# Kernel optimization log

Measured on AMD Instinct MI355X. Metric: run time of the kernel, lower is better.

Reference implementation:

```python
import jax, jax.numpy as jnp
import numpy as np

N_SITES = 1024
A_PER_SITE = 2
R_PER_ALLELE = 16
N_ALLELES = N_SITES * A_PER_SITE
N_READS = N_ALLELES * R_PER_ALLELE
C_IN, C, L = 16, 32, 150


def conv1d(x, w, stride=1, dilation=1, pad=2):
    return jax.lax.conv_general_dilated(
        x, w, (stride,), [(pad, pad)], rhs_dilation=(dilation,),
        dimension_numbers=('NCH', 'OIH', 'NCH'))


def reduce_slots(d, slots):
    # cumsum-diff segmented sum over dim 0, exactly as torch reduceSlots
    res = jnp.cumsum(d, axis=0)
    idx = jnp.cumsum(slots) - 1
    sel = res[idx]
    padded = jnp.concatenate([jnp.zeros_like(sel[:1]), sel[:-1]], axis=0)
    return sel - padded


def xattn(allele, site0, site1, wq, wk, wv, wo):
    # cross-attention: allele features query the two expanded site-feature streams
    q = jnp.einsum('oc,ncl->nol', wq, allele)
    kv = jnp.concatenate([site0, site1], axis=-1)  # [Na, C, 2*L']
    k = jnp.einsum('oc,ncl->nol', wk, kv)
    v = jnp.einsum('oc,ncl->nol', wv, kv)
    scores = jnp.einsum('ncl,ncm->nlm', q, k) / np.float32(np.sqrt(C))
    ctx = jnp.einsum('nlm,ncm->ncl', jax.nn.softmax(scores, axis=-1), v)
    return jnp.mean(allele + ctx, axis=-1) @ wo.T  # [Na, 2]


def setup_inputs():
    ks = jax.random.split(jax.random.key(0), 24)
    w = lambda i, shape: jax.random.normal(ks[i], shape, jnp.float32) * 0.05
    return {
        'tensors0': jax.random.normal(ks[0], (N_READS, C_IN, L), jnp.float32),
        'tensors1': jax.random.normal(ks[1], (N_READS, C_IN, L), jnp.float32),
        'conv0_w': w(2, (C, C_IN, 5)), 'conv1_w': w(3, (C, C_IN, 5)),
        'comp0_w': w(4, (C, C, 3)), 'comp1_w': w(5, (C, C, 3)), 'comp2_w': w(6, (C, C, 3)),
        'xq0': w(7, (C, C)), 'xk0': w(8, (C, C)), 'xv0': w(9, (C, C)), 'xo0': w(10, (2, C)),
        'xq1': w(11, (C, C)), 'xk1': w(12, (C, C)), 'xv1': w(13, (C, C)), 'xo1': w(14, (2, C)),
        'xq2': w(15, (C, C)), 'xk2': w(16, (C, C)), 'xv2': w(17, (C, C)), 'xo2': w(18, (2, C)),
        'comb_w': w(19, (C, 2 * C)), 'meta_w': w(20, (3, 2 * C)), 'meta_b': w(21, (3,)),
        'num_alleles_per_site': jnp.full((N_SITES,), A_PER_SITE, jnp.int32),
        'num_reads0': jnp.full((N_ALLELES,), R_PER_ALLELE, jnp.int32),
        'num_reads1': jnp.full((N_ALLELES,), R_PER_ALLELE, jnp.int32),
    }


def reference(tensors0, tensors1, conv0_w, conv1_w, comp0_w, comp1_w, comp2_w,
              xq0, xk0, xv0, xo0, xq1, xk1, xv1, xo1, xq2, xk2, xv2, xo2,
              comb_w, meta_w, meta_b, num_alleles_per_site, num_reads0, num_reads1):
    compressor = lambda x, w: jax.nn.relu(conv1d(x, w, stride=2, dilation=2, pad=2))

    def compress_and_predict(red_allele, comp_w, xw):
        cfa = compressor(red_allele, comp_w)                       # [Na, C, L']
        rfs = reduce_slots(red_allele, num_alleles_per_site)       # [Ns, C, L]
        cfs0 = compressor(rfs, comp_w)                             # [Ns, C, L']
        exp0 = jnp.repeat(cfs0, num_alleles_per_site, axis=0, total_repeat_length=N_ALLELES)
        cfs1 = reduce_slots(cfa, num_alleles_per_site)             # [Ns, C, L']
        exp1 = jnp.repeat(cfs1, num_alleles_per_site, axis=0, total_repeat_length=N_ALLELES)
        return xattn(cfa, exp0, exp1, *xw), (cfs0, cfs1)

    rc0 = jax.nn.relu(conv1d(tensors0, conv0_w, pad=2))            # [Nr, C, L]
    red0 = reduce_slots(rc0, num_reads0)                           # [Na, C, L]
    e0, _ = compress_and_predict(red0, comp0_w, (xq0, xk0, xv0, xo0))

    rc1 = jax.nn.relu(conv1d(tensors1, conv1_w, pad=2))
    red1 = reduce_slots(rc1, num_reads1)
    e1, _ = compress_and_predict(red1, comp1_w, (xq1, xk1, xv1, xo1))

    red2 = jax.nn.relu(jnp.einsum('oc,ncl->nol', comb_w, jnp.concatenate([red0, red1], axis=1)))
    e2, (s0, s1) = compress_and_predict(red2, comp2_w, (xq2, xk2, xv2, xo2))

    meta_feat = jnp.mean(jnp.concatenate([s0, s1], axis=1), axis=-1)  # [Ns, 2C]
    meta = jax.nn.softmax(meta_feat @ meta_w.T + meta_b, axis=-1)     # [Ns, 3]
    return (jnp.stack([e0, e1, e2]), meta)
```

## Files before the change

### kernel.cpp

```cpp
#include <hip/hip_runtime.h>
#include <math.h>

#define NS 1024
#define NA 2048
#define CIN 16
#define CC 32
#define LL 150
#define LC 75

typedef __attribute__((ext_vector_type(8))) short short8;
typedef __attribute__((ext_vector_type(4))) float float4v;

__device__ __forceinline__ unsigned short f2bf(float f) {
  unsigned int u = __float_as_uint(f);
  unsigned int r = (u + 0x7FFFu + ((u >> 16) & 1u)) >> 16;
  return (unsigned short)r;
}

__device__ __forceinline__ unsigned int pkbf(float lo, float hi) {
  return (unsigned int)f2bf(lo) | ((unsigned int)f2bf(hi) << 16);
}

__device__ __forceinline__ float bflo(unsigned int u) { return __uint_as_float(u << 16); }
__device__ __forceinline__ float bfhi(unsigned int u) { return __uint_as_float(u & 0xffff0000u); }

#if __has_builtin(__builtin_amdgcn_fdot2_f32_bf16)
typedef __attribute__((ext_vector_type(2))) __bf16 bf16x2;
__device__ __forceinline__ float bdot2(unsigned int a, unsigned int b, float c) {
  return __builtin_amdgcn_fdot2_f32_bf16(__builtin_bit_cast(bf16x2, a),
                                         __builtin_bit_cast(bf16x2, b), c, false);
}
#else
__device__ __forceinline__ float bdot2(unsigned int a, unsigned int b, float c) {
  return c + bflo(a) * bflo(b) + bfhi(a) * bfhi(b);
}
#endif

__global__ __launch_bounds__(256) void k_conv_sum_mfma(const float* __restrict__ x,
                                                       const float* __restrict__ w,
                                                       float* __restrict__ red) {
  __shared__ unsigned short xs[2][154 * 32];
  const int a = blockIdx.x;
  const int tid = threadIdx.x;
  const int lane = tid & 63;
  const int wv = tid >> 6;

  short8 afr[2][3];
  {
    const int mrow = lane & 15;
    const int h = lane >> 4;
    for (int mt = 0; mt < 2; ++mt) {
      const int c = mt * 16 + mrow;
      for (int s = 0; s < 3; ++s) {
        short8 f;
#pragma unroll
        for (int j = 0; j < 8; ++j) {
          int ic = 4 * h + (j >> 1);
          int tap = 2 * s + (j & 1);
          float wval = (tap < 5) ? w[c * 80 + ic * 5 + tap] : 0.f;
          f[j] = (short)f2bf(wval);
        }
        afr[mt][s] = f;
      }
    }
  }

  float4v sum[2][3];
#pragma unroll
  for (int mt = 0; mt < 2; ++mt)
#pragma unroll
    for (int nt = 0; nt < 3; ++nt) sum[mt][nt] = (float4v)(0.f);

  const int nbase = wv * 48;
  const int nrow = lane & 15;
  const int hh = lane >> 4;
  const float4v zf = (float4v)(0.f);

  auto stage = [&](int r, int buf) {
    const float* xr = x + (size_t)(a * 16 + r) * (CIN * LL);
    unsigned int* xb32 = (unsigned int*)xs[buf];
    for (int idx = tid; idx < 16 * 38; idx += 256) {
      const int ic = idx & 15;
      const int seg = idx >> 4;
      const int l0 = seg * 4;
      const float* row = xr + ic * LL;
      float v0, v1, v2, v3, v4;
      if (seg < 37) {
        float2 u = *(const float2*)(row + l0);
        float2 u2 = *(const float2*)(row + l0 + 2);
        v0 = u.x; v1 = u.y; v2 = u2.x; v3 = u2.y;
        v4 = row[l0 + 4];
      } else {
        float2 u = *(const float2*)(row + 148);
        v0 = u.x; v1 = u.y; v2 = 0.f; v3 = 0.f; v4 = 0.f;
      }
      const int hb = 4 * (ic >> 2) + (ic & 3);
      unsigned int* b32 = xb32 + 16 * (l0 + 2) + hb;
      b32[0]  = pkbf(v0, v1);
      b32[16] = pkbf(v1, v2);
      b32[32] = pkbf(v2, v3);
      b32[48] = pkbf(v3, v4);
    }
    if (tid < 32) {
      const int ic = tid & 15;
      const int which = tid >> 4;
      const int hb = 4 * (ic >> 2) + (ic & 3);
      xb32[16 * which + hb] = which ? pkbf(0.f, xr[ic * LL]) : 0u;
    }
  };

  stage(0, 0);
  __syncthreads();

  for (int r = 0; r < 16; ++r) {
    const int cur = r & 1;
    if (r + 1 < 16) stage(r + 1, cur ^ 1);

    float4v acc[2][3];
#pragma unroll
    for (int s = 0; s < 3; ++s) {
#pragma unroll
      for (int nt = 0; nt < 3; ++nt) {
        int p = nbase + nt * 16 + nrow + 2 * s;
        if (p >= 154) p -= 154;
        short8 bfrag = *(const short8*)&xs[cur][(4 * p + hh) * 8];
#pragma unroll
        for (int mt = 0; mt < 2; ++mt) {
          acc[mt][nt] = __builtin_amdgcn_mfma_f32_16x16x32_bf16(
              afr[mt][s], bfrag, (s == 0) ? zf : acc[mt][nt], 0, 0, 0);
        }
      }
    }
#pragma unroll
    for (int mt = 0; mt < 2; ++mt)
#pragma unroll
      for (int nt = 0; nt < 3; ++nt)
#pragma unroll
        for (int q = 0; q < 4; ++q) sum[mt][nt][q] += fmaxf(acc[mt][nt][q], 0.f);

    __syncthreads();
  }

  const int ccol = lane & 15;
  const int crow4 = (lane >> 4) * 4;
  for (int mt = 0; mt < 2; ++mt)
    for (int nt = 0; nt < 3; ++nt) {
      int l = nbase + nt * 16 + ccol;
      if (l < LL) {
#pragma unroll
        for (int q = 0; q < 4; ++q) {
          int c = mt * 16 + crow4 + q;
          red[(size_t)a * (CC * LL) + c * LL + l] = sum[mt][nt][q];
        }
      }
    }
}

__global__ __launch_bounds__(256) void k_comb(const float* __restrict__ red0,
                                              const float* __restrict__ red1,
                                              const float* __restrict__ cw,
                                              float* __restrict__ out) {
  __shared__ float ins[64][152];
  __shared__ float cwl[64][CC];
  const int a = blockIdx.x;
  const int tid = threadIdx.x;

  for (int i = tid; i < 64 * CC; i += 256) {
    int c = i & 31; int c2 = i >> 5;
    cwl[c2][c] = cw[c * 64 + c2];
  }
  for (int i = tid; i < CC * LL; i += 256) {
    int c2 = i / LL; int l = i - c2 * LL;
    ins[c2][l] = red0[(size_t)a * (CC * LL) + i];
    ins[32 + c2][l] = red1[(size_t)a * (CC * LL) + i];
  }
  __syncthreads();

  const int c = tid & 31;
  const int lg = tid >> 5;
  const int l0 = lg * 19;
  const int nl = (LL - l0 < 19) ? (LL - l0) : 19;
  float v[19];
#pragma unroll
  for (int j = 0; j < 19; ++j) v[j] = 0.f;
  for (int c2 = 0; c2 < 64; ++c2) {
    float wv = cwl[c2][c];
#pragma unroll
    for (int j = 0; j < 19; ++j) v[j] += wv * ins[c2][l0 + j];
  }
  float* o = out + (size_t)a * (CC * LL) + c * LL + l0;
  for (int j = 0; j < nl; ++j) o[j] = fmaxf(v[j], 0.f);
}

#define AKV_US 0
#define BWK    2400
#define BWV    3456
#define BWQ    4512
#define QT_US  4800
#define BPART  3600
#define BMS    4112
#define CF0_US 11136
#define CF1_US 13536
#define KB_US  15936
#define VB_US  20864
#define ARENA  13056
#define FIN0   0
#define FIN1   4928
#define FWS    9856

__device__ __forceinline__ void attn_phase_d(float* __restrict__ ar, int g, int t,
                                             float& ms) {
  unsigned short* aru = (unsigned short*)ar;
  const float scale = 0.17677669529663687f;
  const int rb_us = (g < 6) ? g * 760 : 9024 + (g - 6) * 760;
#pragma unroll 1
  for (int cc = 0; cc < 2; ++cc) {
    const int ch = g + 8 * cc;
    if (ch >= 15) break;
    const int r0 = ch * 5;

    float2 acc[5][3];
#pragma unroll
    for (int i = 0; i < 5; ++i)
#pragma unroll
      for (int u = 0; u < 3; ++u) acc[i][u] = make_float2(0.f, 0.f);

#pragma unroll 1
    for (int c2 = 0; c2 < 32; c2 += 2) {
      float2 q01[5];
#pragma unroll
      for (int i = 0; i < 5; ++i) {
        unsigned int qp = *(const unsigned int*)&aru[QT_US + (r0 + i) * 32 + c2];
        q01[i] = make_float2(bflo(qp), bfhi(qp));
      }
      const int k0 = KB_US + c2 * 154 + 2 * t;
      const int k1 = k0 + 154;
      unsigned int a0 = *(const unsigned int*)&aru[k0];
      unsigned int a1 = *(const unsigned int*)&aru[k0 + 64];
      unsigned int a2 = *(const unsigned int*)&aru[k0 + 128];
      unsigned int b0 = *(const unsigned int*)&aru[k1];
      unsigned int b1 = *(const unsigned int*)&aru[k1 + 64];
      unsigned int b2 = *(const unsigned int*)&aru[k1 + 128];
      float ka0x = bflo(a0), ka0y = bfhi(a0);
      float ka1x = bflo(a1), ka1y = bfhi(a1);
      float ka2x = bflo(a2), ka2y = bfhi(a2);
      float kb0x = bflo(b0), kb0y = bfhi(b0);
      float kb1x = bflo(b1), kb1y = bfhi(b1);
      float kb2x = bflo(b2), kb2y = bfhi(b2);
#pragma unroll
      for (int i = 0; i < 5; ++i) {
        acc[i][0].x += q01[i].x * ka0x + q01[i].y * kb0x;
        acc[i][0].y += q01[i].x * ka0y + q01[i].y * kb0y;
        acc[i][1].x += q01[i].x * ka1x + q01[i].y * kb1x;
        acc[i][1].y += q01[i].x * ka1y + q01[i].y * kb1y;
        acc[i][2].x += q01[i].x * ka2x + q01[i].y * kb2x;
        acc[i][2].y += q01[i].x * ka2y + q01[i].y * kb2y;
      }
    }

    float inv[5];
#pragma unroll
    for (int i = 0; i < 5; ++i) {
      float s0x = acc[i][0].x * scale, s0y = acc[i][0].y * scale;
      float s1x = acc[i][1].x * scale, s1y = acc[i][1].y * scale;
      float s2x = acc[i][2].x * scale, s2y = acc[i][2].y * scale;
      if (t >= 11) { s2x = -1e30f; s2y = -1e30f; }
      float mx = fmaxf(fmaxf(fmaxf(s0x, s0y), fmaxf(s1x, s1y)), fmaxf(s2x, s2y));
#pragma unroll
      for (int off = 16; off > 0; off >>= 1) mx = fmaxf(mx, __shfl_xor(mx, off, 32));
      float p0x = __expf(s0x - mx), p0y = __expf(s0y - mx);
      float p1x = __expf(s1x - mx), p1y = __expf(s1y - mx);
      float p2x = __expf(s2x - mx), p2y = __expf(s2y - mx);
      float ss = p0x + p0y + p1x + p1y + p2x + p2y;
#pragma unroll
      for (int off = 16; off > 0; off >>= 1) ss += __shfl_xor(ss, off, 32);
      inv[i] = 1.f / ss;
      const int rw = rb_us + i * 152 + 2 * t;
      *(unsigned int*)&aru[rw]      = pkbf(p0x, p0y);
      *(unsigned int*)&aru[rw + 64] = pkbf(p1x, p1y);
      if (t <= 11) *(unsigned int*)&aru[rw + 128] = pkbf(p2x, p2y);
    }

    float pv[5] = {0.f, 0.f, 0.f, 0.f, 0.f};
    const int vb = VB_US + t * 164;
    for (int mq = 0; mq < 38; ++mq) {
      uint2 vv = *(const uint2*)&aru[vb + 4 * mq];
#pragma unroll
      for (int i = 0; i < 5; ++i) {
        uint2 pp = *(const uint2*)&aru[rb_us + i * 152 + 4 * mq];
        pv[i] = bdot2(pp.x, vv.x, pv[i]);
        pv[i] = bdot2(pp.y, vv.y, pv[i]);
      }
    }
#pragma unroll
    for (int i = 0; i < 5; ++i) ms += pv[i] * inv[i];
  }
}

__global__ __launch_bounds__(256) void k_cattn(const float* __restrict__ red,
                                               const float* __restrict__ cw,
                                               const float* __restrict__ wq,
                                               const float* __restrict__ wk,
                                               const float* __restrict__ wv,
                                               const float* __restrict__ wo,
                                               float* __restrict__ cfa,
                                               float* __restrict__ cfs,
                                               float* __restrict__ eout,
                                               int wg) {
  __shared__ float ar[ARENA];
  unsigned short* aru = (unsigned short*)ar;
  const int s = blockIdx.x;
  const int tid = threadIdx.x;
  const int g = tid >> 5;
  const int t = tid & 31;

  float* a0g = cfa + (size_t)(2 * s) * (CC * LC);
  float* a1g = a0g + CC * LC;
  float* sgw = cfs + (size_t)s * (CC * LC);

  for (int i = tid; i < CC * 3 * CC; i += 256) {
    int c = i & 31; int kk = i >> 5;
    ar[FWS + kk * 32 + c] = cw[c * (CC * 3) + kk];
  }
  if (tid < CC) {
    ar[FIN0 + tid * 154 + 0] = 0.f; ar[FIN0 + tid * 154 + 1] = 0.f;
    ar[FIN0 + tid * 154 + 152] = 0.f; ar[FIN0 + tid * 154 + 153] = 0.f;
    ar[FIN1 + tid * 154 + 0] = 0.f; ar[FIN1 + tid * 154 + 1] = 0.f;
    ar[FIN1 + tid * 154 + 152] = 0.f; ar[FIN1 + tid * 154 + 153] = 0.f;
  }
  {
    const float* s0 = red + (size_t)(2 * s) * (CC * LL);
    const float* s1 = s0 + CC * LL;
    for (int i = tid; i < CC * LL; i += 256) {
      int ic = i / LL; int l = i - ic * LL;
      ar[FIN0 + ic * 154 + l + 2] = s0[i];
      ar[FIN1 + ic * 154 + l + 2] = s1[i];
    }
  }
  __syncthreads();

  const int j0 = g * 10;
  const int nj = (LC - j0 < 10) ? (LC - j0) : 10;
  float v0[10], v1[10];
#pragma unroll
  for (int j = 0; j < 10; ++j) { v0[j] = 0.f; v1[j] = 0.f; }
  for (int ic = 0; ic < CC; ++ic) {
    float w0 = ar[FWS + (ic * 3 + 0) * 32 + t];
    float w1 = ar[FWS + (ic * 3 + 1) * 32 + t];
    float w2 = ar[FWS + (ic * 3 + 2) * 32 + t];
    float xa[12], xb[12];
#pragma unroll
    for (int i = 0; i < 12; ++i) {
      xa[i] = ar[FIN0 + ic * 154 + 2 * j0 + 2 * i];
      xb[i] = ar[FIN1 + ic * 154 + 2 * j0 + 2 * i];
    }
#pragma unroll
    for (int j = 0; j < 10; ++j) {
      v0[j] += w0 * xa[j] + w1 * xa[j + 1] + w2 * xa[j + 2];
      v1[j] += w0 * xb[j] + w1 * xb[j + 1] + w2 * xb[j + 2];
    }
  }
  __syncthreads();

  for (int j = 0; j < nj; ++j) {
    const int jj = j0 + j;
    float r0 = fmaxf(v0[j], 0.f);
    float r1 = fmaxf(v1[j], 0.f);
    float cs = fmaxf(v0[j] + v1[j], 0.f);
    aru[AKV_US + jj * 32 + t]        = f2bf(cs);
    aru[AKV_US + (75 + jj) * 32 + t] = f2bf(r0 + r1);
    aru[CF0_US + jj * 32 + t]        = f2bf(r0);
    aru[CF1_US + jj * 32 + t]        = f2bf(r1);
    if (wg) {
      a0g[t * 75 + jj] = r0;
      a1g[t * 75 + jj] = r1;
      sgw[t * 75 + jj] = cs;
    }
  }
  for (int i = tid; i < CC * CC; i += 256) {
    int o = i >> 5, ii = i & 31;
    ar[BWQ + ii * 33 + o] = wq[i];
    ar[BWK + ii * 33 + o] = wk[i];
    ar[BWV + ii * 33 + o] = wv[i];
  }
  __syncthreads();

  unsigned int wq2[16], wk2[16], wv2[16];
  {
    float wqc[32], wkc[32], wvc[32];
#pragma unroll
    for (int ii = 0; ii < 32; ++ii) {
      wqc[ii] = ar[BWQ + ii * 33 + t];
      wkc[ii] = ar[BWK + ii * 33 + t];
      wvc[ii] = ar[BWV + ii * 33 + t];
    }
#pragma unroll
    for (int j = 0; j < 16; ++j) {
      wq2[j] = pkbf(wqc[2 * j], wqc[2 * j + 1]);
      wk2[j] = pkbf(wkc[2 * j], wkc[2 * j + 1]);
      wv2[j] = pkbf(wvc[2 * j], wvc[2 * j + 1]);
    }
  }
  __syncthreads();

  float cfp0 = 0.f;
  for (int row = g; row < 75; row += 8) {
    const unsigned int* cr = (const unsigned int*)&aru[CF0_US + row * 32];
    float acc = 0.f;
#pragma unroll
    for (int j = 0; j < 16; ++j) acc = bdot2(wq2[j], cr[j], acc);
    aru[QT_US + row * 32 + t] = f2bf(acc);
    cfp0 += bflo((unsigned int)aru[CF0_US + row * 32 + t]);
  }
  __syncthreads();

  {
    for (int idx = tid; idx < CC * LL; idx += 256) {
      int o = idx & 31, m = idx >> 5;
      const unsigned int* kvrow = (const unsigned int*)&aru[AKV_US + m * 32];
      float ka = 0.f, va = 0.f;
#pragma unroll
      for (int j = 0; j < 16; ++j) {
        unsigned int u = kvrow[j];
        ka = bdot2(wk2[j], u, ka);
        va = bdot2(wv2[j], u, va);
      }
      aru[KB_US + o * 154 + m] = f2bf(ka);
      aru[VB_US + o * 164 + m] = f2bf(va);
    }
    if (tid < 32) *(unsigned int*)&aru[VB_US + tid * 164 + 150] = 0u;
  }
  __syncthreads();

  float ms0 = 0.f;
  attn_phase_d(ar, g, t, ms0);
  __syncthreads();

  float cfp1 = 0.f;
  for (int row = g; row < 75; row += 8) {
    const unsigned int* cr = (const unsigned int*)&aru[CF1_US + row * 32];
    float acc = 0.f;
#pragma unroll
    for (int j = 0; j < 16; ++j) acc = bdot2(wq2[j], cr[j], acc);
    aru[QT_US + row * 32 + t] = f2bf(acc);
    cfp1 += bflo((unsigned int)aru[CF1_US + row * 32 + t]);
  }
  __syncthreads();

  float ms1 = 0.f;
  attn_phase_d(ar, g, t, ms1);
  __syncthreads();

  ar[BPART + g * 32 + t]       = cfp0 + ms0;
  ar[BPART + 256 + g * 32 + t] = cfp1 + ms1;
  __syncthreads();

  if (tid < 64) {
    int al = tid >> 5, tt = tid & 31;
    float tot = 0.f;
#pragma unroll
    for (int gg = 0; gg < 8; ++gg) tot += ar[BPART + al * 256 + gg * 32 + tt];
    ar[BMS + al * 32 + tt] = tot * (1.f / 75.f);
  }
  __syncthreads();
  if (tid < 4) {
    int al = tid >> 1, o2 = tid & 1;
    float e = 0.f;
#pragma unroll
    for (int c2 = 0; c2 < CC; ++c2) e += wo[o2 * CC + c2] * ar[BMS + al * 32 + c2];
    eout[s * 4 + tid] = e;
  }
}

__global__ __launch_bounds__(64) void k_meta(const float* __restrict__ cfs0,
                                             const float* __restrict__ cfa2,
                                             const float* __restrict__ mw,
                                             const float* __restrict__ mb,
                                             float* __restrict__ mout) {
  __shared__ float feat[64];
  __shared__ float lgt[3];
  const int s = blockIdx.x;
  const int tid = threadIdx.x;
  float f = 0.f;
  if (tid < 32) {
    const float* p = cfs0 + (size_t)s * (CC * LC) + tid * LC;
    for (int l = 0; l < LC; ++l) f += p[l];
  } else {
    const float* p0 = cfa2 + (size_t)(2 * s) * (CC * LC) + (tid - 32) * LC;
    const float* p1 = cfa2 + (size_t)(2 * s + 1) * (CC * LC) + (tid - 32) * LC;
    for (int l = 0; l < LC; ++l) f += p0[l] + p1[l];
  }
  feat[tid] = f * (1.f / 75.f);
  __syncthreads();
  if (tid < 3) {
    float acc2 = mb[tid];
    for (int c2 = 0; c2 < 64; ++c2) acc2 += mw[tid * 64 + c2] * feat[c2];
    lgt[tid] = acc2;
  }
  __syncthreads();
  if (tid < 3) {
    float mx = fmaxf(lgt[0], fmaxf(lgt[1], lgt[2]));
    float e0 = __expf(lgt[0] - mx), e1 = __expf(lgt[1] - mx), e2 = __expf(lgt[2] - mx);
    mout[s * 3 + tid] = __expf(lgt[tid] - mx) / (e0 + e1 + e2);
  }
}

extern "C" void kernel_launch(void* const* d_in, const int* in_sizes, int n_in,
                              void* d_out, int out_size, void* d_ws, size_t ws_size,
                              hipStream_t stream) {
  const float* t0      = (const float*)d_in[0];
  const float* t1      = (const float*)d_in[1];
  const float* conv0_w = (const float*)d_in[2];
  const float* conv1_w = (const float*)d_in[3];
  const float* comp0_w = (const float*)d_in[4];
  const float* comp1_w = (const float*)d_in[5];
  const float* comp2_w = (const float*)d_in[6];
  const float* xq0 = (const float*)d_in[7];
  const float* xk0 = (const float*)d_in[8];
  const float* xv0 = (const float*)d_in[9];
  const float* xo0 = (const float*)d_in[10];
  const float* xq1 = (const float*)d_in[11];
  const float* xk1 = (const float*)d_in[12];
  const float* xv1 = (const float*)d_in[13];
  const float* xo1 = (const float*)d_in[14];
  const float* xq2 = (const float*)d_in[15];
  const float* xk2 = (const float*)d_in[16];
  const float* xv2 = (const float*)d_in[17];
  const float* xo2 = (const float*)d_in[18];
  const float* comb_w = (const float*)d_in[19];
  const float* meta_w = (const float*)d_in[20];
  const float* meta_b = (const float*)d_in[21];

  float* wsf  = (float*)d_ws;
  float* red0 = wsf;
  float* red1 = red0 + (size_t)NA * CC * LL;
  float* cfa  = red1 + (size_t)NA * CC * LL;
  float* cfs0 = cfa + (size_t)NA * CC * LC;
  float* out  = (float*)d_out;

  k_conv_sum_mfma<<<NA, 256, 0, stream>>>(t0, conv0_w, red0);
  k_conv_sum_mfma<<<NA, 256, 0, stream>>>(t1, conv1_w, red1);

  k_cattn<<<NS, 256, 0, stream>>>(red0, comp0_w, xq0, xk0, xv0, xo0,
                                  cfa, cfs0, out + 0, 0);
  k_cattn<<<NS, 256, 0, stream>>>(red1, comp1_w, xq1, xk1, xv1, xo1,
                                  cfa, cfs0, out + 2 * NA, 0);

  k_comb<<<NA, 256, 0, stream>>>(red0, red1, comb_w, red0);
  k_cattn<<<NS, 256, 0, stream>>>(red0, comp2_w, xq2, xk2, xv2, xo2,
                                  cfa, cfs0, out + 4 * NA, 1);

  k_meta<<<NS, 64, 0, stream>>>(cfs0, cfa, meta_w, meta_b, out + 6 * NA);
}
```

Baseline: 1.204 ms.

## Stage conv inputs via coalesced raw bf16 LDS copy with two-deep prefetch

Each read's input is now loaded with coalesced float4 global loads, converted to bf16 and written into a raw LDS buffer. A separate LDS-to-LDS pass then builds the tap-interleaved layout that feeds the MFMA B fragments. Raw copies run two reads ahead and the layout build one read ahead. The goal is fewer scattered global loads and more latency hiding in the conv+sum kernel. The cost is extra LDS capacity and an additional LDS read/write pass per read.

```diff
diff --git a/kernel.cpp b/kernel.cpp
--- a/kernel.cpp
+++ b/kernel.cpp
@@ -40,6 +40,7 @@
                                                        const float* __restrict__ w,
                                                        float* __restrict__ red) {
   __shared__ unsigned short xs[2][154 * 32];
+  __shared__ unsigned short rawB[2][CIN * LL];
   const int a = blockIdx.x;
   const int tid = threadIdx.x;
   const int lane = tid & 63;
@@ -76,45 +77,49 @@
   const int hh = lane >> 4;
   const float4v zf = (float4v)(0.f);
 
-  auto stage = [&](int r, int buf) {
-    const float* xr = x + (size_t)(a * 16 + r) * (CIN * LL);
-    unsigned int* xb32 = (unsigned int*)xs[buf];
-    for (int idx = tid; idx < 16 * 38; idx += 256) {
-      const int ic = idx & 15;
-      const int seg = idx >> 4;
-      const int l0 = seg * 4;
-      const float* row = xr + ic * LL;
-      float v0, v1, v2, v3, v4;
-      if (seg < 37) {
-        float2 u = *(const float2*)(row + l0);
-        float2 u2 = *(const float2*)(row + l0 + 2);
-        v0 = u.x; v1 = u.y; v2 = u2.x; v3 = u2.y;
-        v4 = row[l0 + 4];
-      } else {
-        float2 u = *(const float2*)(row + 148);
-        v0 = u.x; v1 = u.y; v2 = 0.f; v3 = 0.f; v4 = 0.f;
-      }
-      const int hb = 4 * (ic >> 2) + (ic & 3);
-      unsigned int* b32 = xb32 + 16 * (l0 + 2) + hb;
-      b32[0]  = pkbf(v0, v1);
-      b32[16] = pkbf(v1, v2);
-      b32[32] = pkbf(v2, v3);
-      b32[48] = pkbf(v3, v4);
-    }
-    if (tid < 32) {
-      const int ic = tid & 15;
-      const int which = tid >> 4;
-      const int hb = 4 * (ic >> 2) + (ic & 3);
-      xb32[16 * which + hb] = which ? pkbf(0.f, xr[ic * LL]) : 0u;
+  auto copyraw = [&](int r, int rb) {
+    const float4* xr4 = (const float4*)(x + (size_t)(a * 16 + r) * (CIN * LL));
+    unsigned short* raw = rawB[rb];
+    for (int i = tid; i < 600; i += 256) {
+      float4 u = xr4[i];
+      uint2 d;
+      d.x = pkbf(u.x, u.y);
+      d.y = pkbf(u.z, u.w);
+      *(uint2*)&raw[i * 4] = d;
     }
   };
 
-  stage(0, 0);
+  auto build = [&](int rb, int sb) {
+    const unsigned short* raw = rawB[rb];
+    unsigned int* dst = (unsigned int*)xs[sb];
+    for (int s = tid; s < 616; s += 256) {
+      const int p = s >> 2;
+      const int h4 = (s & 3) * 4;
+      const bool qa = (p >= 2) && (p <= 151);
+      const bool qb = (p >= 1) && (p <= 150);
+      uint4 dw;
+      unsigned int v[4];
+#pragma unroll
+      for (int c = 0; c < 4; ++c) {
+        const int base = (h4 + c) * LL;
+        unsigned int va = qa ? (unsigned int)raw[base + p - 2] : 0u;
+        unsigned int vb = qb ? (unsigned int)raw[base + p - 1] : 0u;
+        v[c] = va | (vb << 16);
+      }
+      dw.x = v[0]; dw.y = v[1]; dw.z = v[2]; dw.w = v[3];
+      *(uint4*)&dst[s * 4] = dw;
+    }
+  };
+
+  copyraw(0, 0);
+  __syncthreads();
+  copyraw(1, 1);
+  build(0, 0);
   __syncthreads();
 
   for (int r = 0; r < 16; ++r) {
-    const int cur = r & 1;
-    if (r + 1 < 16) stage(r + 1, cur ^ 1);
+    if (r + 2 < 16) copyraw(r + 2, r & 1);
+    if (r + 1 < 16) build((r + 1) & 1, (r + 1) & 1);
 
     float4v acc[2][3];
 #pragma unroll
@@ -123,7 +128,7 @@
       for (int nt = 0; nt < 3; ++nt) {
         int p = nbase + nt * 16 + nrow + 2 * s;
         if (p >= 154) p -= 154;
-        short8 bfrag = *(const short8*)&xs[cur][(4 * p + hh) * 8];
+        short8 bfrag = *(const short8*)&xs[r & 1][(4 * p + hh) * 8];
 #pragma unroll
         for (int mt = 0; mt < 2; ++mt) {
           acc[mt][nt] = __builtin_amdgcn_mfma_f32_16x16x32_bf16(
```

Result: no change. 1.203 ms (-0.1%).
